# Performance work log

Measured on AMD Instinct MI355X. Metric: run time of the kernel, lower is better.

The kernel has to match this reference:

```python
import jax, jax.numpy as jnp
import numpy as np

LN_EPS = 1e-5


def setup_inputs() -> dict:
    key = jax.random.key(0)
    ks = jax.random.split(key, 4)
    B, S, H, R = 8, 4096, 1024, 64
    hidden_states = jax.random.normal(ks[0], (B, S, H), dtype=jnp.float32)
    w_down = jax.random.normal(ks[1], (H, R), dtype=jnp.float32) * (1.0 / np.sqrt(H))
    b_down = jnp.zeros((R,), dtype=jnp.float32)
    w_up = jax.random.normal(ks[2], (R, H), dtype=jnp.float32) * (1.0 / np.sqrt(R))
    b_up = jnp.zeros((H,), dtype=jnp.float32)
    ln_gamma = jnp.ones((H,), dtype=jnp.float32)
    ln_beta = jnp.zeros((H,), dtype=jnp.float32)
    return {
        "hidden_states": hidden_states,
        "ln_gamma": ln_gamma,
        "ln_beta": ln_beta,
        "w_down": w_down,
        "b_down": b_down,
        "w_up": w_up,
        "b_up": b_up,
    }


def _layernorm(x, gamma, beta):
    mu = jnp.mean(x, axis=-1, keepdims=True)
    var = jnp.mean(jnp.square(x - mu), axis=-1, keepdims=True)
    return (x - mu) * jax.lax.rsqrt(var + LN_EPS) * gamma + beta


def reference(hidden_states, ln_gamma, ln_beta, w_down, b_down, w_up, b_up):
    # pre-norm adapter: LN -> down-proj -> gelu -> up-proj -> +residual
    res = hidden_states
    h = _layernorm(hidden_states, ln_gamma, ln_beta)
    h = jnp.einsum("bsh,hr->bsr", h, w_down) + b_down
    h = jax.nn.gelu(h, approximate=False)  # torch GELU (exact erf form)
    h = jnp.einsum("bsr,rh->bsh", h, w_up) + b_up
    return h + res
```

## Files before the change

### kernel.cpp

```cpp
#include <hip/hip_runtime.h>
#include <hip/hip_bf16.h>
#include <math.h>

#define H 1024
#define R 64
#define NTHREADS 256
#define ROWS_PER_WAVE 16
#define ROWS_PER_BLOCK 64
#define TSTRIDE 72

typedef __attribute__((ext_vector_type(8))) short short8;
typedef __attribute__((ext_vector_type(4))) float floatx4;

__device__ __forceinline__ unsigned short f2bf(float f) {
    unsigned int u = __builtin_bit_cast(unsigned int, f);
    u += 0x7fffu + ((u >> 16) & 1u);
    return (unsigned short)(u >> 16);
}

__global__ void prep_weights(const float* __restrict__ w_down,
                             const float* __restrict__ w_up,
                             const float* __restrict__ gamma,
                             unsigned short* __restrict__ wsd,
                             unsigned short* __restrict__ wsu) {
    int tid = blockIdx.x * blockDim.x + threadIdx.x;
    int j    = tid & 7;
    int lane = (tid >> 3) & 63;
    int f    = tid >> 9;
    int b = lane >> 4, p = lane & 15;
    {
        int kk = f >> 2, n = f & 3;
        int row = kk * 32 + b * 8 + j;
        int col = n * 16 + p;
        wsd[tid] = f2bf(gamma[row] * w_down[row * R + col]);
    }
    {
        int ks = f >> 6, n = f & 63;
        int row = ks * 32 + b * 8 + j;
        int col = n * 16 + p;
        wsu[tid] = f2bf(w_up[row * H + col]);
    }
}

__global__ void prep_vec(const float* __restrict__ w_down,
                         const float* __restrict__ gamma,
                         const float* __restrict__ beta,
                         const float* __restrict__ b_down,
                         float* __restrict__ w1, float* __restrict__ c0) {
    int r = blockIdx.x;
    int t = threadIdx.x;
    float a = 0.f, c = 0.f;
    for (int h = t; h < H; h += NTHREADS) {
        float wd = w_down[h * R + r];
        a += gamma[h] * wd;
        c += beta[h] * wd;
    }
    #pragma unroll
    for (int off = 32; off >= 1; off >>= 1) {
        a += __shfl_xor(a, off);
        c += __shfl_xor(c, off);
    }
    __shared__ float red[8];
    int wv = t >> 6;
    if ((t & 63) == 0) { red[wv] = a; red[4 + wv] = c; }
    __syncthreads();
    if (t == 0) {
        w1[r] = red[0] + red[1] + red[2] + red[3];
        c0[r] = red[4] + red[5] + red[6] + red[7] + b_down[r];
    }
}

__global__ __launch_bounds__(NTHREADS, 4)
void adapter_kernel(const float* __restrict__ x,
                    const float* __restrict__ b_up,
                    const unsigned short* __restrict__ wsd,
                    const unsigned short* __restrict__ wsu,
                    const float* __restrict__ w1v,
                    const float* __restrict__ c0v,
                    float* __restrict__ out) {
    __shared__ __align__(16) unsigned short t_lds[4][ROWS_PER_WAVE * TSTRIDE];

    const int tid  = threadIdx.x;
    const int lane = tid & 63;
    const int w    = tid >> 6;
    const int p    = lane & 15;
    const int b    = lane >> 4;
    const long row0 = (long)blockIdx.x * ROWS_PER_BLOCK + w * ROWS_PER_WAVE;

    float s1 = 0.f, s2 = 0.f;
    floatx4 acc[4];
    #pragma unroll
    for (int nt = 0; nt < 4; ++nt) acc[nt] = floatx4{0.f, 0.f, 0.f, 0.f};

    const short8* wsd8 = (const short8*)wsd;
    const float* xw = x + (row0 + p) * H + b * 8;
    #pragma unroll 4
    for (int kt = 0; kt < 32; ++kt) {
        floatx4 v0 = *(const floatx4*)(xw + kt * 32);
        floatx4 v1 = *(const floatx4*)(xw + kt * 32 + 4);
        short8 a;
        #pragma unroll
        for (int e = 0; e < 4; ++e) {
            s1 += v0[e] + v1[e];
            s2 += v0[e] * v0[e] + v1[e] * v1[e];
            a[e]     = (short)f2bf(v0[e]);
            a[4 + e] = (short)f2bf(v1[e]);
        }
        #pragma unroll
        for (int nt = 0; nt < 4; ++nt)
            acc[nt] = __builtin_amdgcn_mfma_f32_16x16x32_bf16(a, wsd8[(size_t)(kt * 4 + nt) * 64 + lane], acc[nt], 0, 0, 0);
    }

    s1 += __shfl_xor(s1, 16); s1 += __shfl_xor(s1, 32);
    s2 += __shfl_xor(s2, 16); s2 += __shfl_xor(s2, 32);
    float mu = s1 * (1.0f / (float)H);
    float var = s2 * (1.0f / (float)H) - mu * mu;
    float rs = rsqrtf(var + 1e-5f);

    #pragma unroll
    for (int reg = 0; reg < 4; ++reg) {
        float mur = __shfl(mu, b * 4 + reg);
        float rsr = __shfl(rs, b * 4 + reg);
        #pragma unroll
        for (int nt = 0; nt < 4; ++nt) {
            int col = nt * 16 + p;
            float u = rsr * (acc[nt][reg] - mur * w1v[col]) + c0v[col];
            u = 0.5f * u * (1.0f + erff(u * 0.70710678f));
            t_lds[w][(b * 4 + reg) * TSTRIDE + col] = f2bf(u);
        }
    }
    __syncthreads();

    short8 a0 = *(const short8*)&t_lds[w][p * TSTRIDE + b * 8];
    short8 a1 = *(const short8*)&t_lds[w][p * TSTRIDE + 32 + b * 8];
    const short8* wsu8 = (const short8*)wsu;
    const long rbase = row0 + b * 4;

    #pragma unroll 4
    for (int n = 0; n < 64; ++n) {
        short8 bu0 = wsu8[(size_t)n * 64 + lane];
        short8 bu1 = wsu8[(size_t)(64 + n) * 64 + lane];
        floatx4 av = {0.f, 0.f, 0.f, 0.f};
        av = __builtin_amdgcn_mfma_f32_16x16x32_bf16(a0, bu0, av, 0, 0, 0);
        av = __builtin_amdgcn_mfma_f32_16x16x32_bf16(a1, bu1, av, 0, 0, 0);
        int col = n * 16 + p;
        float bup = b_up[col];
        #pragma unroll
        for (int reg = 0; reg < 4; ++reg) {
            long rr = rbase + reg;
            out[rr * H + col] = av[reg] + bup + x[rr * H + col];
        }
    }
}

extern "C" void kernel_launch(void* const* d_in, const int* in_sizes, int n_in,
                              void* d_out, int out_size, void* d_ws, size_t ws_size,
                              hipStream_t stream) {
    const float* x      = (const float*)d_in[0];
    const float* gamma  = (const float*)d_in[1];
    const float* beta   = (const float*)d_in[2];
    const float* w_down = (const float*)d_in[3];
    const float* b_down = (const float*)d_in[4];
    const float* w_up   = (const float*)d_in[5];
    const float* b_up   = (const float*)d_in[6];
    float* out = (float*)d_out;

    unsigned short* wsd = (unsigned short*)d_ws;
    unsigned short* wsu = wsd + 65536;
    float* w1 = (float*)(wsu + 65536);
    float* c0 = w1 + 64;

    int M = in_sizes[0] / H;
    prep_weights<<<256, 256, 0, stream>>>(w_down, w_up, gamma, wsd, wsu);
    prep_vec<<<64, 256, 0, stream>>>(w_down, gamma, beta, b_down, w1, c0);
    adapter_kernel<<<M / ROWS_PER_BLOCK, NTHREADS, 0, stream>>>(x, b_up, wsd, wsu, w1, c0, out);
}
```

Measured before the change: 289.2 us.

## Software-pipeline loads in adapter kernel and merge prep kernels

Both GEMM phases of the adapter kernel now prefetch their operands into register ring buffers: x and down-projection weights eight and two steps ahead, and up-projection weights, bias and residual values eight columns ahead. This is meant to hide global memory latency behind MFMA work. The two weight-prep kernels are fused into one launch to cut launch overhead. Launch bounds drop to 2 blocks per SM so the larger register footprint fits, at the cost of lower occupancy.

```diff
diff --git a/kernel.cpp b/kernel.cpp
--- a/kernel.cpp
+++ b/kernel.cpp
@@ -5,8 +5,6 @@
 #define H 1024
 #define R 64
 #define NTHREADS 256
-#define ROWS_PER_WAVE 16
-#define ROWS_PER_BLOCK 64
 #define TSTRIDE 72
 
 typedef __attribute__((ext_vector_type(8))) short short8;
@@ -18,59 +16,59 @@
     return (unsigned short)(u >> 16);
 }
 
-__global__ void prep_weights(const float* __restrict__ w_down,
-                             const float* __restrict__ w_up,
-                             const float* __restrict__ gamma,
-                             unsigned short* __restrict__ wsd,
-                             unsigned short* __restrict__ wsu) {
-    int tid = blockIdx.x * blockDim.x + threadIdx.x;
-    int j    = tid & 7;
-    int lane = (tid >> 3) & 63;
-    int f    = tid >> 9;
-    int b = lane >> 4, p = lane & 15;
-    {
-        int kk = f >> 2, n = f & 3;
-        int row = kk * 32 + b * 8 + j;
-        int col = n * 16 + p;
-        wsd[tid] = f2bf(gamma[row] * w_down[row * R + col]);
-    }
-    {
-        int ks = f >> 6, n = f & 63;
-        int row = ks * 32 + b * 8 + j;
-        int col = n * 16 + p;
-        wsu[tid] = f2bf(w_up[row * H + col]);
-    }
-}
-
-__global__ void prep_vec(const float* __restrict__ w_down,
-                         const float* __restrict__ gamma,
-                         const float* __restrict__ beta,
-                         const float* __restrict__ b_down,
-                         float* __restrict__ w1, float* __restrict__ c0) {
-    int r = blockIdx.x;
-    int t = threadIdx.x;
-    float a = 0.f, c = 0.f;
-    for (int h = t; h < H; h += NTHREADS) {
-        float wd = w_down[h * R + r];
-        a += gamma[h] * wd;
-        c += beta[h] * wd;
-    }
-    #pragma unroll
-    for (int off = 32; off >= 1; off >>= 1) {
-        a += __shfl_xor(a, off);
-        c += __shfl_xor(c, off);
-    }
+__global__ void prep(const float* __restrict__ w_down,
+                     const float* __restrict__ w_up,
+                     const float* __restrict__ gamma,
+                     const float* __restrict__ beta,
+                     const float* __restrict__ b_down,
+                     unsigned short* __restrict__ wsd,
+                     unsigned short* __restrict__ wsu,
+                     float* __restrict__ w1, float* __restrict__ c0) {
     __shared__ float red[8];
-    int wv = t >> 6;
-    if ((t & 63) == 0) { red[wv] = a; red[4 + wv] = c; }
-    __syncthreads();
-    if (t == 0) {
-        w1[r] = red[0] + red[1] + red[2] + red[3];
-        c0[r] = red[4] + red[5] + red[6] + red[7] + b_down[r];
-    }
-}
-
-__global__ __launch_bounds__(NTHREADS, 4)
+    int bid = blockIdx.x;
+    if (bid < 256) {
+        int tid = bid * NTHREADS + threadIdx.x;
+        int j    = tid & 7;
+        int lane = (tid >> 3) & 63;
+        int f    = tid >> 9;
+        int b = lane >> 4, p = lane & 15;
+        {
+            int kk = f >> 2, n = f & 3;
+            int row = kk * 32 + b * 8 + j;
+            int col = n * 16 + p;
+            wsd[tid] = f2bf(gamma[row] * w_down[row * R + col]);
+        }
+        {
+            int ks = f >> 6, n = f & 63;
+            int row = ks * 32 + b * 8 + j;
+            int col = n * 16 + p;
+            wsu[tid] = f2bf(w_up[row * H + col]);
+        }
+    } else {
+        int r = bid - 256;
+        int t = threadIdx.x;
+        float a = 0.f, c = 0.f;
+        for (int h = t; h < H; h += NTHREADS) {
+            float wd = w_down[h * R + r];
+            a += gamma[h] * wd;
+            c += beta[h] * wd;
+        }
+        #pragma unroll
+        for (int off = 32; off >= 1; off >>= 1) {
+            a += __shfl_xor(a, off);
+            c += __shfl_xor(c, off);
+        }
+        int wv = t >> 6;
+        if ((t & 63) == 0) { red[wv] = a; red[4 + wv] = c; }
+        __syncthreads();
+        if (t == 0) {
+            w1[r] = red[0] + red[1] + red[2] + red[3];
+            c0[r] = red[4] + red[5] + red[6] + red[7] + b_down[r];
+        }
+    }
+}
+
+__global__ __launch_bounds__(NTHREADS, 2)
 void adapter_kernel(const float* __restrict__ x,
                     const float* __restrict__ b_up,
                     const unsigned short* __restrict__ wsd,
@@ -78,26 +76,73 @@
                     const float* __restrict__ w1v,
                     const float* __restrict__ c0v,
                     float* __restrict__ out) {
-    __shared__ __align__(16) unsigned short t_lds[4][ROWS_PER_WAVE * TSTRIDE];
+    __shared__ __align__(16) unsigned short t_lds[4][16 * TSTRIDE];
 
     const int tid  = threadIdx.x;
     const int lane = tid & 63;
     const int w    = tid >> 6;
     const int p    = lane & 15;
     const int b    = lane >> 4;
-    const long row0 = (long)blockIdx.x * ROWS_PER_BLOCK + w * ROWS_PER_WAVE;
+    const long row0 = (long)blockIdx.x * 64 + w * 16;
 
     float s1 = 0.f, s2 = 0.f;
     floatx4 acc[4];
     #pragma unroll
     for (int nt = 0; nt < 4; ++nt) acc[nt] = floatx4{0.f, 0.f, 0.f, 0.f};
 
+    const float* xw = x + (row0 + p) * H + b * 8;
     const short8* wsd8 = (const short8*)wsd;
-    const float* xw = x + (row0 + p) * H + b * 8;
-    #pragma unroll 4
-    for (int kt = 0; kt < 32; ++kt) {
-        floatx4 v0 = *(const floatx4*)(xw + kt * 32);
-        floatx4 v1 = *(const floatx4*)(xw + kt * 32 + 4);
+
+    floatx4 bx0[8], bx1[8];
+    short8 wd[2][4];
+    #pragma unroll
+    for (int i = 0; i < 8; ++i) {
+        bx0[i] = *(const floatx4*)(xw + i * 32);
+        bx1[i] = *(const floatx4*)(xw + i * 32 + 4);
+    }
+    #pragma unroll
+    for (int nt = 0; nt < 4; ++nt) {
+        wd[0][nt] = wsd8[(size_t)nt * 64 + lane];
+        wd[1][nt] = wsd8[(size_t)(4 + nt) * 64 + lane];
+    }
+
+    for (int ko = 0; ko < 3; ++ko) {
+        #pragma unroll
+        for (int ki = 0; ki < 8; ++ki) {
+            const int kt = ko * 8 + ki;
+            floatx4 v0 = bx0[ki], v1 = bx1[ki];
+            bx0[ki] = *(const floatx4*)(xw + (kt + 8) * 32);
+            bx1[ki] = *(const floatx4*)(xw + (kt + 8) * 32 + 4);
+            short8 wl[4];
+            #pragma unroll
+            for (int nt = 0; nt < 4; ++nt) {
+                wl[nt] = wd[ki & 1][nt];
+                wd[ki & 1][nt] = wsd8[(size_t)((kt + 2) * 4 + nt) * 64 + lane];
+            }
+            short8 a;
+            #pragma unroll
+            for (int e = 0; e < 4; ++e) {
+                s1 += v0[e] + v1[e];
+                s2 += v0[e] * v0[e] + v1[e] * v1[e];
+                a[e]     = (short)f2bf(v0[e]);
+                a[4 + e] = (short)f2bf(v1[e]);
+            }
+            #pragma unroll
+            for (int nt = 0; nt < 4; ++nt)
+                acc[nt] = __builtin_amdgcn_mfma_f32_16x16x32_bf16(a, wl[nt], acc[nt], 0, 0, 0);
+        }
+    }
+    #pragma unroll
+    for (int ki = 0; ki < 8; ++ki) {
+        const int kt = 24 + ki;
+        floatx4 v0 = bx0[ki], v1 = bx1[ki];
+        short8 wl[4];
+        #pragma unroll
+        for (int nt = 0; nt < 4; ++nt) {
+            wl[nt] = wd[ki & 1][nt];
+            if (ki < 6)
+                wd[ki & 1][nt] = wsd8[(size_t)((kt + 2) * 4 + nt) * 64 + lane];
+        }
         short8 a;
         #pragma unroll
         for (int e = 0; e < 4; ++e) {
@@ -108,7 +153,7 @@
         }
         #pragma unroll
         for (int nt = 0; nt < 4; ++nt)
-            acc[nt] = __builtin_amdgcn_mfma_f32_16x16x32_bf16(a, wsd8[(size_t)(kt * 4 + nt) * 64 + lane], acc[nt], 0, 0, 0);
+            acc[nt] = __builtin_amdgcn_mfma_f32_16x16x32_bf16(a, wl[nt], acc[nt], 0, 0, 0);
     }
 
     s1 += __shfl_xor(s1, 16); s1 += __shfl_xor(s1, 32);
@@ -129,27 +174,64 @@
             t_lds[w][(b * 4 + reg) * TSTRIDE + col] = f2bf(u);
         }
     }
+
+    const short8* wsu8 = (const short8*)wsu;
+    const long rbase = row0 + b * 4;
+    short8 wq0[8], wq1[8];
+    float bb[8], rx0[8], rx1[8], rx2[8], rx3[8];
+    #pragma unroll
+    for (int i = 0; i < 8; ++i) {
+        wq0[i] = wsu8[(size_t)i * 64 + lane];
+        wq1[i] = wsu8[(size_t)(64 + i) * 64 + lane];
+        int col = i * 16 + p;
+        bb[i]  = b_up[col];
+        rx0[i] = x[(rbase + 0) * H + col];
+        rx1[i] = x[(rbase + 1) * H + col];
+        rx2[i] = x[(rbase + 2) * H + col];
+        rx3[i] = x[(rbase + 3) * H + col];
+    }
     __syncthreads();
-
     short8 a0 = *(const short8*)&t_lds[w][p * TSTRIDE + b * 8];
     short8 a1 = *(const short8*)&t_lds[w][p * TSTRIDE + 32 + b * 8];
-    const short8* wsu8 = (const short8*)wsu;
-    const long rbase = row0 + b * 4;
-
-    #pragma unroll 4
-    for (int n = 0; n < 64; ++n) {
-        short8 bu0 = wsu8[(size_t)n * 64 + lane];
-        short8 bu1 = wsu8[(size_t)(64 + n) * 64 + lane];
+
+    for (int no = 0; no < 7; ++no) {
+        #pragma unroll
+        for (int ni = 0; ni < 8; ++ni) {
+            const int n = no * 8 + ni;
+            short8 bu0 = wq0[ni], bu1 = wq1[ni];
+            float bup = bb[ni];
+            float r0 = rx0[ni], r1 = rx1[ni], r2 = rx2[ni], r3 = rx3[ni];
+            const int nc = n + 8;
+            const int colc = nc * 16 + p;
+            wq0[ni] = wsu8[(size_t)nc * 64 + lane];
+            wq1[ni] = wsu8[(size_t)(64 + nc) * 64 + lane];
+            bb[ni]  = b_up[colc];
+            rx0[ni] = x[(rbase + 0) * H + colc];
+            rx1[ni] = x[(rbase + 1) * H + colc];
+            rx2[ni] = x[(rbase + 2) * H + colc];
+            rx3[ni] = x[(rbase + 3) * H + colc];
+            floatx4 av = {0.f, 0.f, 0.f, 0.f};
+            av = __builtin_amdgcn_mfma_f32_16x16x32_bf16(a0, bu0, av, 0, 0, 0);
+            av = __builtin_amdgcn_mfma_f32_16x16x32_bf16(a1, bu1, av, 0, 0, 0);
+            const int col = n * 16 + p;
+            out[(rbase + 0) * H + col] = av[0] + bup + r0;
+            out[(rbase + 1) * H + col] = av[1] + bup + r1;
+            out[(rbase + 2) * H + col] = av[2] + bup + r2;
+            out[(rbase + 3) * H + col] = av[3] + bup + r3;
+        }
+    }
+    #pragma unroll
+    for (int ni = 0; ni < 8; ++ni) {
+        const int n = 56 + ni;
+        short8 bu0 = wq0[ni], bu1 = wq1[ni];
         floatx4 av = {0.f, 0.f, 0.f, 0.f};
         av = __builtin_amdgcn_mfma_f32_16x16x32_bf16(a0, bu0, av, 0, 0, 0);
         av = __builtin_amdgcn_mfma_f32_16x16x32_bf16(a1, bu1, av, 0, 0, 0);
-        int col = n * 16 + p;
-        float bup = b_up[col];
-        #pragma unroll
-        for (int reg = 0; reg < 4; ++reg) {
-            long rr = rbase + reg;
-            out[rr * H + col] = av[reg] + bup + x[rr * H + col];
-        }
+        const int col = n * 16 + p;
+        out[(rbase + 0) * H + col] = av[0] + bb[ni] + rx0[ni];
+        out[(rbase + 1) * H + col] = av[1] + bb[ni] + rx1[ni];
+        out[(rbase + 2) * H + col] = av[2] + bb[ni] + rx2[ni];
+        out[(rbase + 3) * H + col] = av[3] + bb[ni] + rx3[ni];
     }
 }
 
@@ -171,7 +253,7 @@
     float* c0 = w1 + 64;
 
     int M = in_sizes[0] / H;
-    prep_weights<<<256, 256, 0, stream>>>(w_down, w_up, gamma, wsd, wsu);
-    prep_vec<<<64, 256, 0, stream>>>(w_down, gamma, beta, b_down, w1, c0);
-    adapter_kernel<<<M / ROWS_PER_BLOCK, NTHREADS, 0, stream>>>(x, b_up, wsd, wsu, w1, c0, out);
-}
+    prep<<<320, NTHREADS, 0, stream>>>(w_down, w_up, gamma, beta, b_down,
+                                       wsd, wsu, w1, c0);
+    adapter_kernel<<<M / 64, NTHREADS, 0, stream>>>(x, b_up, wsd, wsu, w1, c0, out);
+}
```

New measurement: 278.2 us. 1.04x faster.
